# Optimization experiments

Hardware: AMD Instinct MI355X
Metric: run time of the kernel (lower is better)

The kernel has to match this reference:

```python
import jax, jax.numpy as jnp
import numpy as np

N, E, G = 100000, 400000, 64
IN, H, C = 8, 4, 64
HD = H * C  # 256


def setup_inputs() -> dict:
    key = jax.random.key(0)
    ks = jax.random.split(key, 40)
    f = lambda k, shp, s=0.05: jax.random.normal(k, shp, jnp.float32) * s
    inp = {
        "x": jax.random.normal(ks[0], (N, IN), jnp.float32),
        "edge_attr": jax.random.normal(ks[1], (E, 1), jnp.float32),
        "src": jax.random.randint(ks[2], (E,), 0, N),
        "dst": jax.random.randint(ks[3], (E,), 0, N),
        "batch": jnp.sort(jax.random.randint(ks[4], (N,), 0, G)),
        # encoder Linear(8 -> 64)
        "W_enc": f(ks[5], (IN, C)), "b_enc": jnp.zeros((C,), jnp.float32),
        # GATv2 layer 1: in 64 -> H*C=256
        "g1_Wl": f(ks[6], (C, HD)), "g1_bl": jnp.zeros((HD,), jnp.float32),
        "g1_Wr": f(ks[7], (C, HD)), "g1_br": jnp.zeros((HD,), jnp.float32),
        "g1_We": f(ks[8], (1, HD)),
        "g1_att": f(ks[9], (H, C)),
        "g1_bias": jnp.zeros((HD,), jnp.float32),
        # GATv2 layer 2: in 256 -> 256
        "g2_Wl": f(ks[10], (HD, HD)), "g2_bl": jnp.zeros((HD,), jnp.float32),
        "g2_Wr": f(ks[11], (HD, HD)), "g2_br": jnp.zeros((HD,), jnp.float32),
        "g2_We": f(ks[12], (1, HD)),
        "g2_att": f(ks[13], (H, C)),
        "g2_bias": jnp.zeros((HD,), jnp.float32),
        # post MLP: 256 -> 128 -> LN -> relu -> 128 -> 64 -> relu, head 64 -> 1
        "W_p1": f(ks[14], (HD, 128)), "b_p1": jnp.zeros((128,), jnp.float32),
        "ln_g": jnp.ones((128,), jnp.float32), "ln_b": jnp.zeros((128,), jnp.float32),
        "W_p2": f(ks[15], (128, 64)), "b_p2": jnp.zeros((64,), jnp.float32),
        "W_head": f(ks[16], (64, 1)), "b_head": jnp.zeros((1,), jnp.float32),
    }
    return inp


def gatv2(x, src, dst, e_attr, Wl, bl, Wr, br, We, att, bias):
    """PyG GATv2Conv: score = att . LeakyReLU(xl[src] + xr[dst] + e), scatter-softmax over dst,
    out_i = sum_j alpha_ij * xl[j], concat heads, + bias."""
    n = x.shape[0]
    xl = (x @ Wl + bl).reshape(n, H, C)          # source-side transform
    xr = (x @ Wr + br).reshape(n, H, C)          # target-side transform
    ee = (e_attr @ We).reshape(-1, H, C)         # [E,H,C]
    s = jax.nn.leaky_relu(xl[src] + xr[dst] + ee, 0.2)
    logit = jnp.einsum('ehc,hc->eh', s, att)     # [E,H]
    # numerically-stable scatter softmax over edges sharing a target node
    m = jax.ops.segment_max(logit, dst, num_segments=n)
    m = jnp.where(jnp.isfinite(m), m, 0.0)
    ex = jnp.exp(logit - m[dst])
    den = jax.ops.segment_sum(ex, dst, num_segments=n)
    alpha = ex / (den[dst] + 1e-16)
    out = jax.ops.segment_sum(alpha[:, :, None] * xl[src], dst, num_segments=n)
    return out.reshape(n, HD) + bias


def reference(x, edge_attr, src, dst, batch,
              W_enc, b_enc,
              g1_Wl, g1_bl, g1_Wr, g1_br, g1_We, g1_att, g1_bias,
              g2_Wl, g2_bl, g2_Wr, g2_br, g2_We, g2_att, g2_bias,
              W_p1, b_p1, ln_g, ln_b, W_p2, b_p2, W_head, b_head):
    h = jax.nn.relu(x @ W_enc + b_enc)
    h = jax.nn.relu(gatv2(h, src, dst, edge_attr, g1_Wl, g1_bl, g1_Wr, g1_br, g1_We, g1_att, g1_bias))
    h = jax.nn.relu(gatv2(h, src, dst, edge_attr, g2_Wl, g2_bl, g2_Wr, g2_br, g2_We, g2_att, g2_bias))
    # global mean pool per graph
    sums = jax.ops.segment_sum(h, batch, num_segments=G)
    cnt = jax.ops.segment_sum(jnp.ones((h.shape[0],), h.dtype), batch, num_segments=G)
    p = sums / jnp.maximum(cnt, 1.0)[:, None]
    # post MLP (dropout is identity at inference)
    p = p @ W_p1 + b_p1
    mu = jnp.mean(p, axis=-1, keepdims=True)
    var = jnp.mean((p - mu) ** 2, axis=-1, keepdims=True)
    p = (p - mu) * jax.lax.rsqrt(var + 1e-5) * ln_g + ln_b
    p = jax.nn.relu(p)
    p = jax.nn.relu(p @ W_p2 + b_p2)
    return (p @ W_head + b_head)[:, 0]  # [G]
```

## Files before the change

### kernel.cpp

```cpp
#include <hip/hip_runtime.h>
#include <hip/hip_fp16.h>
#include <math.h>


#define HD 256
#define NHEAD 4
#define CH 64

typedef _Float16 half8 __attribute__((ext_vector_type(8)));
typedef _Float16 h2 __attribute__((ext_vector_type(2)));
typedef __attribute__((ext_vector_type(4))) float f32x4;

__device__ __forceinline__ h2 pack_h2(float a, float b) {
#if __has_builtin(__builtin_amdgcn_cvt_pkrtz)
    return __builtin_bit_cast(h2, __builtin_amdgcn_cvt_pkrtz(a, b));
#else
    return h2{(_Float16)a, (_Float16)b};
#endif
}

__device__ __forceinline__ float fast_exp2(float x) {
#if __has_builtin(__builtin_amdgcn_exp2f)
    return __builtin_amdgcn_exp2f(x);
#else
    return exp2f(x);
#endif
}

__device__ __forceinline__ float dot2f(h2 a, h2 b, float c) {
#if __has_builtin(__builtin_amdgcn_fdot2)
    typedef __fp16 fp16v2 __attribute__((ext_vector_type(2)));
    return __builtin_amdgcn_fdot2(__builtin_bit_cast(fp16v2, a),
                                  __builtin_bit_cast(fp16v2, b), c, false);
#else
    return c + (float)a.x * (float)b.x + (float)a.y * (float)b.y;
#endif
}

__device__ __forceinline__ void prep_one(const float* Wl, const float* Wr,
                                         ushort* frag, int K, int t) {
    int l = t & 63;
    int ct = (t >> 6) & 31;
    int ks = t >> 11;
    int n = l & 15, q = l >> 4;
    const float* W = (ct < 16) ? Wl : Wr;
    int col = (ct & 15) * 16 + n;
    ushort* phi = frag + (size_t)t * 8;
#pragma unroll
    for (int j = 0; j < 8; ++j) {
        int k = ks * 32 + q * 8 + j;
        float wv = W[(size_t)k * 256 + col];
        phi[j] = __half_as_ushort(__float2half(wv));
    }
}

__global__ void setup_kernel(int* __restrict__ zbase, int nzero,
                             const float* __restrict__ Wl1, const float* __restrict__ Wr1,
                             ushort* __restrict__ f1,
                             const float* __restrict__ Wl2, const float* __restrict__ Wr2,
                             ushort* __restrict__ f2) {
    int i = blockIdx.x * 256 + threadIdx.x;
    if (i < nzero) {
        zbase[i] = 0;
    } else {
        int gt = i - nzero;
        if (gt < 64 * 64) prep_one(Wl1, Wr1, f1, 64, gt);
        else if (gt < 64 * 64 + 256 * 64) prep_one(Wl2, Wr2, f2, 256, gt - 64 * 64);
    }
}

__global__ void deg_kernel(const int* __restrict__ dst, int* __restrict__ cnt, int E) {
    int e = blockIdx.x * 256 + threadIdx.x;
    if (e < E) atomicAdd(&cnt[dst[e]], 1);
}

__global__ void scan_block(const int* __restrict__ cnt, int* __restrict__ off,
                           int* __restrict__ bsum, int N) {
    __shared__ int s[256];
    int i = blockIdx.x * 256 + threadIdx.x;
    int v = (i < N) ? cnt[i] : 0;
    s[threadIdx.x] = v;
    __syncthreads();
    for (int d = 1; d < 256; d <<= 1) {
        int t = 0;
        if (threadIdx.x >= d) t = s[threadIdx.x - d];
        __syncthreads();
        s[threadIdx.x] += t;
        __syncthreads();
    }
    if (i < N) off[i + 1] = s[threadIdx.x];
    if (threadIdx.x == 255) bsum[blockIdx.x] = s[255];
    if (blockIdx.x == 0 && threadIdx.x == 0) off[0] = 0;
}

__global__ void scan_add2(int* __restrict__ off, const int* __restrict__ bsum, int N) {
    __shared__ int red[4];
    int b = blockIdx.x;
    int s = 0;
    for (int i = threadIdx.x; i < b; i += 256) s += bsum[i];
    for (int o = 32; o > 0; o >>= 1) s += __shfl_xor(s, o);
    if ((threadIdx.x & 63) == 0) red[threadIdx.x >> 6] = s;
    __syncthreads();
    int prefix = red[0] + red[1] + red[2] + red[3];
    int i = b * 256 + threadIdx.x;
    if (i < N) off[i + 1] += prefix;
}

__global__ void scatter_kernel(const int* __restrict__ dst, const int* __restrict__ src,
                               const float* __restrict__ eattr, const int* __restrict__ off,
                               int* __restrict__ cur, int2* __restrict__ edata, int E) {
    int e = blockIdx.x * 256 + threadIdx.x;
    if (e < E) {
        int d = dst[e];
        int p = atomicAdd(&cur[d], 1);
        edata[off[d] + p] = make_int2(src[e] << 9, __float_as_int(eattr[e]));
    }
}

template <int K, bool FUSE_ENC>
__global__ __launch_bounds__(512, 4) void gemm_mfma(
    const void* Av, const float* __restrict__ Wenc, const float* __restrict__ benc,
    const ushort* __restrict__ Bfrag,
    const float* __restrict__ bl, const float* __restrict__ br,
    ushort* __restrict__ outL, ushort* outR, int N) {
    constexpr int KS = K / 32;
    constexpr int FRAG_SHORTS = KS * 4 * 64 * 8;
    constexpr int TB_STRIDE = 260;
    constexpr int SH_BYTES = (FRAG_SHORTS * 2 > 64 * TB_STRIDE * 2)
                                 ? FRAG_SHORTS * 2 : 64 * TB_STRIDE * 2;
    __shared__ __align__(16) char shraw[SH_BYTES];
    ushort* frag = (ushort*)shraw;
    ushort* tbuf = (ushort*)shraw;

    const int t = threadIdx.x;
    const int row0 = blockIdx.x * 64;
    const float* Ax = (const float*)Av;
    const ushort* Ahalf = (const ushort*)Av;

    const int w = t >> 6, l = t & 63;

    if constexpr (FUSE_ENC) {
        constexpr int C4 = K / 4;
        constexpr int LC4 = 4;
#pragma unroll
        for (int it = 0; it < (64 * C4) / 512; ++it) {
            int jj = it * 512 + t;
            int m = jj & 15;
            int c4 = (jj >> 4) & (C4 - 1);
            int rg = jj >> (4 + LC4);
            int row = row0 + rg * 16 + m;
            ushort4 sv = make_ushort4(0, 0, 0, 0);
            if (row < N) {
                float4 xa = *(const float4*)(Ax + (size_t)row * 8);
                float4 xb = *(const float4*)(Ax + (size_t)row * 8 + 4);
                float xrv[8] = {xa.x, xa.y, xa.z, xa.w, xb.x, xb.y, xb.z, xb.w};
                ushort o[4];
#pragma unroll
                for (int j = 0; j < 4; ++j) {
                    int c = c4 * 4 + j;
                    float a = benc[c];
#pragma unroll
                    for (int u = 0; u < 8; ++u) a = fmaf(xrv[u], Wenc[u * 64 + c], a);
                    o[j] = __half_as_ushort(__float2half(fmaxf(a, 0.f)));
                }
                sv = make_ushort4(o[0], o[1], o[2], o[3]);
            }
            int c = c4 * 4;
            int ks = c >> 5, q = (c >> 3) & 3, jb = c & 7;
            int cell = (ks * 4 + rg) * 64 + m + 16 * q;
            *(ushort4*)(frag + cell * 8 + jb) = sv;
        }
    } else {
#if __has_builtin(__builtin_amdgcn_global_load_lds)
#pragma unroll
        for (int it = 0; it < 4; ++it) {
            int row = row0 + it * 16 + (l & 15);
            const ushort* srcp = Ahalf + (size_t)row * 256 + w * 32 + (l >> 4) * 8;
            ushort* dstp = frag + (size_t)(w * 4 + it) * 64 * 8;
            if (row < N) {
                __builtin_amdgcn_global_load_lds(
                    (const __attribute__((address_space(1))) unsigned int*)srcp,
                    (__attribute__((address_space(3))) unsigned int*)dstp,
                    16, 0, 0);
            }
        }
#else
        constexpr int C8 = K / 8;
        constexpr int LC8 = 5;
#pragma unroll
        for (int it = 0; it < (64 * C8) / 512; ++it) {
            int jj = it * 512 + t;
            int m = jj & 15;
            int c8 = (jj >> 4) & (C8 - 1);
            int rg = jj >> (4 + LC8);
            int row = row0 + rg * 16 + m;
            uint4 sv = make_uint4(0, 0, 0, 0);
            if (row < N) sv = *(const uint4*)(Ahalf + (size_t)row * K + c8 * 8);
            int ks = c8 >> 2, q = c8 & 3;
            int cell = (ks * 4 + rg) * 64 + m + 16 * q;
            *(uint4*)(frag + cell * 8) = sv;
        }
#endif
    }
    __syncthreads();

    const int ct0 = w * 4;

    f32x4 acc[4][4];
#pragma unroll
    for (int rt = 0; rt < 4; ++rt)
#pragma unroll
        for (int c = 0; c < 4; ++c) acc[rt][c] = (f32x4){0.f, 0.f, 0.f, 0.f};

#pragma unroll
    for (int ks = 0; ks < KS; ++ks) {
        half8 a[4];
#pragma unroll
        for (int rt = 0; rt < 4; ++rt) {
            int cell = (ks * 4 + rt) * 64 + l;
            a[rt] = *(const half8*)(frag + cell * 8);
        }
#pragma unroll
        for (int c = 0; c < 4; ++c) {
            size_t e = ((size_t)(ks * 32 + ct0 + c) * 64 + l) * 8;
            half8 bh = *(const half8*)(Bfrag + e);
#pragma unroll
            for (int rt = 0; rt < 4; ++rt)
                acc[rt][c] = __builtin_amdgcn_mfma_f32_16x16x32_f16(a[rt], bh, acc[rt][c], 0, 0, 0);
        }
    }

    const int m = l & 15, q = l >> 4;
#pragma unroll
    for (int half = 0; half < 2; ++half) {
        __syncthreads();
        if ((w >> 2) == half) {
            const float* bias = half ? br : bl;
#pragma unroll
            for (int c = 0; c < 4; ++c) {
                int col = ((ct0 + c) & 15) * 16 + m;
                float bb = bias[col];
#pragma unroll
                for (int rt = 0; rt < 4; ++rt)
#pragma unroll
                    for (int r = 0; r < 4; ++r)
                        tbuf[(rt * 16 + q * 4 + r) * TB_STRIDE + col] =
                            __half_as_ushort(__float2half(acc[rt][c][r] + bb));
            }
        }
        __syncthreads();
        ushort* outp = half ? outR : outL;
#pragma unroll
        for (int it = 0; it < 4; ++it) {
            int jj = it * 512 + t;
            int row = jj >> 5;
            int ch = jj & 31;
            int grow = row0 + row;
            if (grow < N) {
                uint2 a0 = *(const uint2*)(tbuf + row * TB_STRIDE + ch * 8);
                uint2 a1 = *(const uint2*)(tbuf + row * TB_STRIDE + ch * 8 + 4);
                *(uint4*)(outp + (size_t)grow * 256 + ch * 8) =
                    make_uint4(a0.x, a0.y, a1.x, a1.y);
            }
        }
    }
}

__global__ __launch_bounds__(256) void gat_aggregate(
    const ushort* __restrict__ xl, const ushort* xr,
    const int* __restrict__ off, const int2* __restrict__ edata,
    const float* __restrict__ We, const float* __restrict__ att,
    const float* __restrict__ bias, ushort* out, int N) {
    const int wid = blockIdx.x * 4 + (threadIdx.x >> 6);
    if (wid * 2 >= N) return;
    const int lane = threadIdx.x & 63;
    const int l32 = lane & 31;
    const int node = wid * 2 + (lane >> 5);
    const int cbase = (l32 >> 3) * 64 + (l32 & 7) * 8;
    const unsigned cb2 = (unsigned)cbase * 2;

    const float LOG2E = 1.44269504f;
    float4 wf0 = *(const float4*)(We + cbase);
    float4 wf1 = *(const float4*)(We + cbase + 4);
    float4 af0 = *(const float4*)(att + cbase);
    float4 af1 = *(const float4*)(att + cbase + 4);
    h2 we[4], at[4];
    we[0] = pack_h2(wf0.x, wf0.y); we[1] = pack_h2(wf0.z, wf0.w);
    we[2] = pack_h2(wf1.x, wf1.y); we[3] = pack_h2(wf1.z, wf1.w);
    at[0] = pack_h2(af0.x * LOG2E, af0.y * LOG2E);
    at[1] = pack_h2(af0.z * LOG2E, af0.w * LOG2E);
    at[2] = pack_h2(af1.x * LOG2E, af1.y * LOG2E);
    at[3] = pack_h2(af1.z * LOG2E, af1.w * LOG2E);

    const h2 z2 = {(_Float16)0.f, (_Float16)0.f};
    const h2 c02 = {(_Float16)0.2f, (_Float16)0.2f};

    const bool valid = node < N;
    const size_t nb = (size_t)node * HD;
    h2 xrv[4] = {z2, z2, z2, z2};
    int s0i = 0, s1i = 0;
    if (valid) {
        uint4 xu = *(const uint4*)(xr + nb + cbase);
        xrv[0] = __builtin_bit_cast(h2, xu.x);
        xrv[1] = __builtin_bit_cast(h2, xu.y);
        xrv[2] = __builtin_bit_cast(h2, xu.z);
        xrv[3] = __builtin_bit_cast(h2, xu.w);
        s0i = off[node];
        s1i = off[node + 1];
    }

    const char* xlb = (const char*)xl;
    const char* eb = (const char*)edata;
    float l = 0.f;
    h2 acc[4] = {z2, z2, z2, z2};

    int j[4];
    float ea[4];
    {
        unsigned tb = (unsigned)s0i << 3;
        int2 e0 = *(const int2*)(eb + tb);
        int2 e1 = *(const int2*)(eb + tb + 8);
        int2 e2 = *(const int2*)(eb + tb + 16);
        int2 e3 = *(const int2*)(eb + tb + 24);
        j[0] = e0.x; ea[0] = __int_as_float(e0.y);
        j[1] = e1.x; ea[1] = __int_as_float(e1.y);
        j[2] = e2.x; ea[2] = __int_as_float(e2.y);
        j[3] = e3.x; ea[3] = __int_as_float(e3.y);
    }
    int t = s0i;
    while (__any(t < s1i)) {
        int nE = s1i - t;
        int jc[4];
        float eac[4];
#pragma unroll
        for (int u = 0; u < 4; ++u) { jc[u] = j[u]; eac[u] = ea[u]; }
        h2 xv[4][4];
#pragma unroll
        for (int u = 0; u < 4; ++u) {
            unsigned a = (u < nE) ? (unsigned)jc[u] : 0u;
            uint4 xu = *(const uint4*)(xlb + (a + cb2));
            xv[u][0] = __builtin_bit_cast(h2, xu.x);
            xv[u][1] = __builtin_bit_cast(h2, xu.y);
            xv[u][2] = __builtin_bit_cast(h2, xu.z);
            xv[u][3] = __builtin_bit_cast(h2, xu.w);
        }
        {
            unsigned tb = (unsigned)(t + 4) << 3;
            int2 e0 = *(const int2*)(eb + tb);
            int2 e1 = *(const int2*)(eb + tb + 8);
            int2 e2 = *(const int2*)(eb + tb + 16);
            int2 e3 = *(const int2*)(eb + tb + 24);
            j[0] = e0.x; ea[0] = __int_as_float(e0.y);
            j[1] = e1.x; ea[1] = __int_as_float(e1.y);
            j[2] = e2.x; ea[2] = __int_as_float(e2.y);
            j[3] = e3.x; ea[3] = __int_as_float(e3.y);
        }
        float rr[4];
#pragma unroll
        for (int u = 0; u < 4; ++u) {
            _Float16 eh = (_Float16)eac[u];
            h2 e2 = {eh, eh};
            float v = 0.f;
#pragma unroll
            for (int k = 0; k < 4; ++k) {
                h2 s = e2 * we[k] + (xv[u][k] + xrv[k]);
                s = __builtin_elementwise_max(s, z2) + __builtin_elementwise_min(s, z2) * c02;
                v = dot2f(at[k], s, v);
            }
            rr[u] = v;
        }
        h2 r01 = pack_h2(rr[0], rr[1]);
        h2 r23 = pack_h2(rr[2], rr[3]);
#pragma unroll
        for (int o = 1; o <= 4; o <<= 1) {
            int v01 = __shfl_xor(__builtin_bit_cast(int, r01), o);
            int v23 = __shfl_xor(__builtin_bit_cast(int, r23), o);
            r01 = r01 + __builtin_bit_cast(h2, v01);
            r23 = r23 + __builtin_bit_cast(h2, v23);
        }
        float r0 = (float)r01.x, r1 = (float)r01.y;
        float r2 = (float)r23.x, r3 = (float)r23.y;
        if (0 >= nE) r0 = -1e30f;
        if (1 >= nE) r1 = -1e30f;
        if (2 >= nE) r2 = -1e30f;
        if (3 >= nE) r3 = -1e30f;
        float p0 = fast_exp2(r0);
        float p1 = fast_exp2(r1);
        float p2 = fast_exp2(r2);
        float p3 = fast_exp2(r3);
        l += (p0 + p1) + (p2 + p3);
        h2 ph0 = pack_h2(p0, p0);
        h2 ph1 = pack_h2(p1, p1);
        h2 ph2 = pack_h2(p2, p2);
        h2 ph3 = pack_h2(p3, p3);
#pragma unroll
        for (int k = 0; k < 4; ++k) {
            acc[k] = ph0 * xv[0][k] + acc[k];
            acc[k] = ph1 * xv[1][k] + acc[k];
            acc[k] = ph2 * xv[2][k] + acc[k];
            acc[k] = ph3 * xv[3][k] + acc[k];
        }
        t += 4;
    }
    if (valid) {
        float inv = 1.f / (l + 1e-16f);
        float4 b0 = *(const float4*)(bias + cbase);
        float4 b1 = *(const float4*)(bias + cbase + 4);
        float q0 = fmaxf(fmaf((float)acc[0].x, inv, b0.x), 0.f);
        float q1 = fmaxf(fmaf((float)acc[0].y, inv, b0.y), 0.f);
        float q2 = fmaxf(fmaf((float)acc[1].x, inv, b0.z), 0.f);
        float q3 = fmaxf(fmaf((float)acc[1].y, inv, b0.w), 0.f);
        float q4 = fmaxf(fmaf((float)acc[2].x, inv, b1.x), 0.f);
        float q5 = fmaxf(fmaf((float)acc[2].y, inv, b1.y), 0.f);
        float q6 = fmaxf(fmaf((float)acc[3].x, inv, b1.z), 0.f);
        float q7 = fmaxf(fmaf((float)acc[3].y, inv, b1.w), 0.f);
        uint w0 = (uint)__half_as_ushort(__float2half(q0)) |
                  ((uint)__half_as_ushort(__float2half(q1)) << 16);
        uint w1 = (uint)__half_as_ushort(__float2half(q2)) |
                  ((uint)__half_as_ushort(__float2half(q3)) << 16);
        uint w2 = (uint)__half_as_ushort(__float2half(q4)) |
                  ((uint)__half_as_ushort(__float2half(q5)) << 16);
        uint w3 = (uint)__half_as_ushort(__float2half(q6)) |
                  ((uint)__half_as_ushort(__float2half(q7)) << 16);
        *(uint4*)(out + nb + cbase) = make_uint4(w0, w1, w2, w3);
    }
}

__device__ __forceinline__ int lowerb(const int* b, int n, int v) {
    int lo = 0, hi = n;
    while (lo < hi) {
        int mid = (lo + hi) >> 1;
        if (b[mid] < v) lo = mid + 1; else hi = mid;
    }
    return lo;
}

__global__ __launch_bounds__(256) void pool_kernel(
    const ushort* __restrict__ h, const int* __restrict__ batch,
    float* __restrict__ pooled, float* __restrict__ gcnt, int N) {
    const int g = blockIdx.x >> 5, part = blockIdx.x & 31;
    const int start = lowerb(batch, N, g);
    const int end = lowerb(batch, N, g + 1);
    const int rows = end - start;
    const int r0 = start + (int)((long long)rows * part / 32);
    const int r1 = start + (int)((long long)rows * (part + 1) / 32);

    const int slot = threadIdx.x >> 5;
    const int l32 = threadIdx.x & 31;

    float acc[8] = {0.f, 0.f, 0.f, 0.f, 0.f, 0.f, 0.f, 0.f};
    for (int r = r0 + slot; r < r1; r += 8) {
        uint4 v = *(const uint4*)(h + (size_t)r * HD + l32 * 8);
        h2 a0 = __builtin_bit_cast(h2, v.x);
        h2 a1 = __builtin_bit_cast(h2, v.y);
        h2 a2 = __builtin_bit_cast(h2, v.z);
        h2 a3 = __builtin_bit_cast(h2, v.w);
        acc[0] += (float)a0.x; acc[1] += (float)a0.y;
        acc[2] += (float)a1.x; acc[3] += (float)a1.y;
        acc[4] += (float)a2.x; acc[5] += (float)a2.y;
        acc[6] += (float)a3.x; acc[7] += (float)a3.y;
    }
#pragma unroll
    for (int k = 0; k < 8; ++k) acc[k] += __shfl_xor(acc[k], 32);

    __shared__ float sred[4][32][9];
    const int w = threadIdx.x >> 6;
    if ((threadIdx.x & 63) < 32) {
#pragma unroll
        for (int k = 0; k < 8; ++k) sred[w][l32][k] = acc[k];
    }
    __syncthreads();
    {
        const int li = threadIdx.x >> 3;
        const int k = threadIdx.x & 7;
        float s = (sred[0][li][k] + sred[1][li][k]) +
                  (sred[2][li][k] + sred[3][li][k]);
        atomicAdd(&pooled[g * HD + li * 8 + k], s);
    }
    if (part == 0 && threadIdx.x == 0) gcnt[g] = (float)rows;
}

__global__ void mlp_kernel(const float* __restrict__ pooled, const float* __restrict__ gcnt,
                           const float* __restrict__ W_p1, const float* __restrict__ b_p1,
                           const float* __restrict__ ln_g, const float* __restrict__ ln_b,
                           const float* __restrict__ W_p2, const float* __restrict__ b_p2,
                           const float* __restrict__ W_head, const float* __restrict__ b_head,
                           float* __restrict__ out) {
    int g = blockIdx.x;
    int j = threadIdx.x;
    __shared__ float sh[128];
    __shared__ float red[2];

    float inv = 1.f / fmaxf(gcnt[g], 1.f);
    float v = b_p1[j];
    for (int k = 0; k < 256; ++k) v = fmaf(pooled[g * 256 + k] * inv, W_p1[k * 128 + j], v);

    float s = v;
    for (int o = 32; o > 0; o >>= 1) s += __shfl_xor(s, o);
    if ((j & 63) == 0) red[j >> 6] = s;
    __syncthreads();
    float mu = (red[0] + red[1]) * (1.f / 128.f);
    float d = v - mu;
    float s2 = d * d;
    for (int o = 32; o > 0; o >>= 1) s2 += __shfl_xor(s2, o);
    __syncthreads();
    if ((j & 63) == 0) red[j >> 6] = s2;
    __syncthreads();
    float var = (red[0] + red[1]) * (1.f / 128.f);

    float p = d * rsqrtf(var + 1e-5f) * ln_g[j] + ln_b[j];
    sh[j] = fmaxf(p, 0.f);
    __syncthreads();

    if (j < 64) {
        float q = b_p2[j];
        for (int k = 0; k < 128; ++k) q = fmaf(sh[k], W_p2[k * 64 + j], q);
        q = fmaxf(q, 0.f);
        float t = q * W_head[j];
        for (int o = 32; o > 0; o >>= 1) t += __shfl_xor(t, o);
        if (j == 0) out[g] = t + b_head[0];
    }
}

extern "C" void kernel_launch(void* const* d_in, const int* in_sizes, int n_in,
                              void* d_out, int out_size, void* d_ws, size_t ws_size,
                              hipStream_t stream) {
    const float* x      = (const float*)d_in[0];
    const float* eattr  = (const float*)d_in[1];
    const int*   src    = (const int*)d_in[2];
    const int*   dst    = (const int*)d_in[3];
    const int*   batch  = (const int*)d_in[4];
    const float* W_enc  = (const float*)d_in[5];
    const float* b_enc  = (const float*)d_in[6];
    const float* g1_Wl  = (const float*)d_in[7];
    const float* g1_bl  = (const float*)d_in[8];
    const float* g1_Wr  = (const float*)d_in[9];
    const float* g1_br  = (const float*)d_in[10];
    const float* g1_We  = (const float*)d_in[11];
    const float* g1_att = (const float*)d_in[12];
    const float* g1_bias= (const float*)d_in[13];
    const float* g2_Wl  = (const float*)d_in[14];
    const float* g2_bl  = (const float*)d_in[15];
    const float* g2_Wr  = (const float*)d_in[16];
    const float* g2_br  = (const float*)d_in[17];
    const float* g2_We  = (const float*)d_in[18];
    const float* g2_att = (const float*)d_in[19];
    const float* g2_bias= (const float*)d_in[20];
    const float* W_p1   = (const float*)d_in[21];
    const float* b_p1   = (const float*)d_in[22];
    const float* ln_g   = (const float*)d_in[23];
    const float* ln_b   = (const float*)d_in[24];
    const float* W_p2   = (const float*)d_in[25];
    const float* b_p2   = (const float*)d_in[26];
    const float* W_head = (const float*)d_in[27];
    const float* b_head = (const float*)d_in[28];

    const int N = in_sizes[0] / 8;
    const int E = in_sizes[2];

    char* p = (char*)d_ws;
    auto alloc = [&](size_t bytes) -> void* {
        void* r = (void*)p;
        p += (bytes + 255) & ~(size_t)255;
        return r;
    };
    ushort* bufA   = (ushort*)alloc((size_t)N * HD * 2);
    ushort* bufXL  = (ushort*)alloc((size_t)N * HD * 2);
    int*    cnt    = (int*)alloc((size_t)N * 4);
    int*    curp   = (int*)alloc((size_t)N * 4);
    float*  pooled = (float*)alloc(64 * HD * 4);
    char*   zend   = p;
    int*    off    = (int*)alloc((size_t)(N + 1) * 4);
    int2*   edata  = (int2*)alloc((size_t)(E + 8) * 8);
    const int nb   = (N + 255) / 256;
    int*    bsum   = (int*)alloc((size_t)nb * 4);
    float*  gcnt   = (float*)alloc(64 * 4);
    ushort* wfrag1 = (ushort*)alloc((size_t)64 * 64 * 16 * 2);
    ushort* wfrag2 = (ushort*)alloc((size_t)256 * 64 * 16 * 2);

    const int nzero = (int)(((char*)zend - (char*)cnt) / 4);
    const int nsetup = nzero + 64 * 64 + 256 * 64;

    setup_kernel<<<(nsetup + 255) / 256, 256, 0, stream>>>(
        cnt, nzero, g1_Wl, g1_Wr, wfrag1, g2_Wl, g2_Wr, wfrag2);

    deg_kernel<<<(E + 255) / 256, 256, 0, stream>>>(dst, cnt, E);
    scan_block<<<nb, 256, 0, stream>>>(cnt, off, bsum, N);
    scan_add2<<<nb, 256, 0, stream>>>(off, bsum, N);
    scatter_kernel<<<(E + 255) / 256, 256, 0, stream>>>(dst, src, eattr, off, curp,
                                                        edata, E);

    const int gblocks = (N + 63) / 64;
    const int ablocks = (N + 7) / 8;

    gemm_mfma<64, true><<<gblocks, 512, 0, stream>>>(
        x, W_enc, b_enc, wfrag1, g1_bl, g1_br, bufXL, bufA, N);
    gat_aggregate<<<ablocks, 256, 0, stream>>>(
        bufXL, bufA, off, edata, g1_We, g1_att, g1_bias, bufA, N);

    gemm_mfma<256, false><<<gblocks, 512, 0, stream>>>(
        bufA, nullptr, nullptr, wfrag2, g2_bl, g2_br, bufXL, bufA, N);
    gat_aggregate<<<ablocks, 256, 0, stream>>>(
        bufXL, bufA, off, edata, g2_We, g2_att, g2_bias, bufA, N);

    pool_kernel<<<64 * 32, 256, 0, stream>>>(bufA, batch, pooled, gcnt, N);
    mlp_kernel<<<64, 128, 0, stream>>>(pooled, gcnt, W_p1, b_p1, ln_g, ln_b,
                                       W_p2, b_p2, W_head, b_head, (float*)d_out);
}
```

Before: 358.0 us.

## Sort nodes by in-degree to balance edges across aggregate wavefronts

Adds a counting sort of nodes by in-degree (histogram, scan, scatter into a permutation), and the GAT aggregation kernels process nodes in that permuted order. Each wavefront handles two nodes on half-waves, so pairing nodes of similar degree is meant to cut divergence and idle lanes from degree imbalance. The cost is three extra small kernels plus an indirection through perm, which makes the xr reads and output writes non-contiguous across neighbouring waves and can hurt coalescing and cache locality.

```diff
diff --git a/kernel.cpp b/kernel.cpp
--- a/kernel.cpp
+++ b/kernel.cpp
@@ -115,6 +115,42 @@
         int p = atomicAdd(&cur[d], 1);
         edata[off[d] + p] = make_int2(src[e] << 9, __float_as_int(eattr[e]));
     }
+}
+
+__global__ void dhist_kernel(const int* __restrict__ cnt, int* __restrict__ dhist, int N) {
+    __shared__ int lh[64];
+    if (threadIdx.x < 64) lh[threadIdx.x] = 0;
+    __syncthreads();
+    int i = blockIdx.x * 256 + threadIdx.x;
+    if (i < N) atomicAdd(&lh[min(cnt[i], 63)], 1);
+    __syncthreads();
+    if (threadIdx.x < 64 && lh[threadIdx.x] > 0)
+        atomicAdd(&dhist[threadIdx.x], lh[threadIdx.x]);
+}
+
+__global__ void dscan_kernel(const int* __restrict__ dhist, int* __restrict__ dcur) {
+    if (threadIdx.x == 0) {
+        int a = 0;
+        for (int k = 0; k < 64; ++k) { dcur[k] = a; a += dhist[k]; }
+    }
+}
+
+__global__ void sort_scatter(const int* __restrict__ cnt, int* __restrict__ dcur,
+                             int* __restrict__ perm, int N) {
+    __shared__ int lh[64], lbase[64];
+    if (threadIdx.x < 64) lh[threadIdx.x] = 0;
+    __syncthreads();
+    int i = blockIdx.x * 256 + threadIdx.x;
+    int bin = 0, r = 0;
+    if (i < N) {
+        bin = min(cnt[i], 63);
+        r = atomicAdd(&lh[bin], 1);
+    }
+    __syncthreads();
+    if (threadIdx.x < 64 && lh[threadIdx.x] > 0)
+        lbase[threadIdx.x] = atomicAdd(&dcur[threadIdx.x], lh[threadIdx.x]);
+    __syncthreads();
+    if (i < N) perm[lbase[bin] + r] = i;
 }
 
 template <int K, bool FUSE_ENC>
@@ -269,13 +305,14 @@
 __global__ __launch_bounds__(256) void gat_aggregate(
     const ushort* __restrict__ xl, const ushort* xr,
     const int* __restrict__ off, const int2* __restrict__ edata,
+    const int* __restrict__ perm,
     const float* __restrict__ We, const float* __restrict__ att,
     const float* __restrict__ bias, ushort* out, int N) {
     const int wid = blockIdx.x * 4 + (threadIdx.x >> 6);
     if (wid * 2 >= N) return;
     const int lane = threadIdx.x & 63;
     const int l32 = lane & 31;
-    const int node = wid * 2 + (lane >> 5);
+    const int idx = wid * 2 + (lane >> 5);
     const int cbase = (l32 >> 3) * 64 + (l32 & 7) * 8;
     const unsigned cb2 = (unsigned)cbase * 2;
 
@@ -295,7 +332,9 @@
     const h2 z2 = {(_Float16)0.f, (_Float16)0.f};
     const h2 c02 = {(_Float16)0.2f, (_Float16)0.2f};
 
-    const bool valid = node < N;
+    const bool valid = idx < N;
+    int node = 0;
+    if (valid) node = perm[idx];
     const size_t nb = (size_t)node * HD;
     h2 xrv[4] = {z2, z2, z2, z2};
     int s0i = 0, s1i = 0;
@@ -568,6 +607,7 @@
     ushort* bufXL  = (ushort*)alloc((size_t)N * HD * 2);
     int*    cnt    = (int*)alloc((size_t)N * 4);
     int*    curp   = (int*)alloc((size_t)N * 4);
+    int*    dhist  = (int*)alloc(64 * 4);
     float*  pooled = (float*)alloc(64 * HD * 4);
     char*   zend   = p;
     int*    off    = (int*)alloc((size_t)(N + 1) * 4);
@@ -575,6 +615,8 @@
     const int nb   = (N + 255) / 256;
     int*    bsum   = (int*)alloc((size_t)nb * 4);
     float*  gcnt   = (float*)alloc(64 * 4);
+    int*    dcur   = (int*)alloc(64 * 4);
+    int*    perm   = (int*)alloc((size_t)N * 4);
     ushort* wfrag1 = (ushort*)alloc((size_t)64 * 64 * 16 * 2);
     ushort* wfrag2 = (ushort*)alloc((size_t)256 * 64 * 16 * 2);
 
@@ -585,8 +627,11 @@
         cnt, nzero, g1_Wl, g1_Wr, wfrag1, g2_Wl, g2_Wr, wfrag2);
 
     deg_kernel<<<(E + 255) / 256, 256, 0, stream>>>(dst, cnt, E);
+    dhist_kernel<<<nb, 256, 0, stream>>>(cnt, dhist, N);
+    dscan_kernel<<<1, 64, 0, stream>>>(dhist, dcur);
     scan_block<<<nb, 256, 0, stream>>>(cnt, off, bsum, N);
     scan_add2<<<nb, 256, 0, stream>>>(off, bsum, N);
+    sort_scatter<<<nb, 256, 0, stream>>>(cnt, dcur, perm, N);
     scatter_kernel<<<(E + 255) / 256, 256, 0, stream>>>(dst, src, eattr, off, curp,
                                                         edata, E);
 
@@ -596,12 +641,12 @@
     gemm_mfma<64, true><<<gblocks, 512, 0, stream>>>(
         x, W_enc, b_enc, wfrag1, g1_bl, g1_br, bufXL, bufA, N);
     gat_aggregate<<<ablocks, 256, 0, stream>>>(
-        bufXL, bufA, off, edata, g1_We, g1_att, g1_bias, bufA, N);
+        bufXL, bufA, off, edata, perm, g1_We, g1_att, g1_bias, bufA, N);
 
     gemm_mfma<256, false><<<gblocks, 512, 0, stream>>>(
         bufA, nullptr, nullptr, wfrag2, g2_bl, g2_br, bufXL, bufA, N);
     gat_aggregate<<<ablocks, 256, 0, stream>>>(
-        bufXL, bufA, off, edata, g2_We, g2_att, g2_bias, bufA, N);
+        bufXL, bufA, off, edata, perm, g2_We, g2_att, g2_bias, bufA, N);
 
     pool_kernel<<<64 * 32, 256, 0, stream>>>(bufA, batch, pooled, gcnt, N);
     mlp_kernel<<<64, 128, 0, stream>>>(pooled, gcnt, W_p1, b_p1, ln_g, ln_b,
```

Result: slower. 377.3 us (+5.4%).

## Add 32-row MFMA GEMM kernel for layer-2 transform with wider column tiles

Applied to the files above, without the earlier changes.

Replaces the layer-2 GEMM (256->512 outputs) with a dedicated kernel that processes 32 rows per block using 256 threads. Each wave computes 8 column tiles over 2 row tiles, so each B fragment loaded from global memory feeds two MFMAs. The kernel writes both the left and right halves in a single epilogue pass. The intent is to double the grid size and shrink per-block shared memory for better occupancy and latency hiding, at the cost of more B-fragment traffic per output row. The generic kernel's non-fused branch is removed since only the fused-encoder instantiation remains.

```diff
diff --git a/kernel.cpp b/kernel.cpp
--- a/kernel.cpp
+++ b/kernel.cpp
@@ -135,11 +135,10 @@
     const int t = threadIdx.x;
     const int row0 = blockIdx.x * 64;
     const float* Ax = (const float*)Av;
-    const ushort* Ahalf = (const ushort*)Av;
 
     const int w = t >> 6, l = t & 63;
 
-    if constexpr (FUSE_ENC) {
+    {
         constexpr int C4 = K / 4;
         constexpr int LC4 = 4;
 #pragma unroll
@@ -170,37 +169,6 @@
             int cell = (ks * 4 + rg) * 64 + m + 16 * q;
             *(ushort4*)(frag + cell * 8 + jb) = sv;
         }
-    } else {
-#if __has_builtin(__builtin_amdgcn_global_load_lds)
-#pragma unroll
-        for (int it = 0; it < 4; ++it) {
-            int row = row0 + it * 16 + (l & 15);
-            const ushort* srcp = Ahalf + (size_t)row * 256 + w * 32 + (l >> 4) * 8;
-            ushort* dstp = frag + (size_t)(w * 4 + it) * 64 * 8;
-            if (row < N) {
-                __builtin_amdgcn_global_load_lds(
-                    (const __attribute__((address_space(1))) unsigned int*)srcp,
-                    (__attribute__((address_space(3))) unsigned int*)dstp,
-                    16, 0, 0);
-            }
-        }
-#else
-        constexpr int C8 = K / 8;
-        constexpr int LC8 = 5;
-#pragma unroll
-        for (int it = 0; it < (64 * C8) / 512; ++it) {
-            int jj = it * 512 + t;
-            int m = jj & 15;
-            int c8 = (jj >> 4) & (C8 - 1);
-            int rg = jj >> (4 + LC8);
-            int row = row0 + rg * 16 + m;
-            uint4 sv = make_uint4(0, 0, 0, 0);
-            if (row < N) sv = *(const uint4*)(Ahalf + (size_t)row * K + c8 * 8);
-            int ks = c8 >> 2, q = c8 & 3;
-            int cell = (ks * 4 + rg) * 64 + m + 16 * q;
-            *(uint4*)(frag + cell * 8) = sv;
-        }
-#endif
     }
     __syncthreads();
 
@@ -262,6 +230,105 @@
                 *(uint4*)(outp + (size_t)grow * 256 + ch * 8) =
                     make_uint4(a0.x, a0.y, a1.x, a1.y);
             }
+        }
+    }
+}
+
+__global__ __launch_bounds__(256, 4) void gemm_mfma32(
+    const ushort* __restrict__ A, const ushort* __restrict__ Bfrag,
+    const float* __restrict__ bl, const float* __restrict__ br,
+    ushort* __restrict__ outL, ushort* outR, int N) {
+    constexpr int TB_STRIDE = 516;
+    constexpr int SH_BYTES = 32 * TB_STRIDE * 2;
+    __shared__ __align__(16) char shraw[SH_BYTES];
+    ushort* frag = (ushort*)shraw;
+    ushort* tbuf = (ushort*)shraw;
+
+    const int t = threadIdx.x;
+    const int row0 = blockIdx.x * 32;
+    const int w = t >> 6, l = t & 63;
+
+#if __has_builtin(__builtin_amdgcn_global_load_lds)
+#pragma unroll
+    for (int it = 0; it < 4; ++it) {
+        int cb = w * 4 + it;
+        int ks = cb >> 1, rg = cb & 1;
+        int row = row0 + rg * 16 + (l & 15);
+        const ushort* srcp = A + (size_t)row * 256 + ks * 32 + (l >> 4) * 8;
+        ushort* dstp = frag + (size_t)cb * 512;
+        if (row < N) {
+            __builtin_amdgcn_global_load_lds(
+                (const __attribute__((address_space(1))) unsigned int*)srcp,
+                (__attribute__((address_space(3))) unsigned int*)dstp,
+                16, 0, 0);
+        }
+    }
+#else
+#pragma unroll
+    for (int it = 0; it < 4; ++it) {
+        int cb = w * 4 + it;
+        int ks = cb >> 1, rg = cb & 1;
+        int row = row0 + rg * 16 + (l & 15);
+        uint4 sv = make_uint4(0, 0, 0, 0);
+        if (row < N) sv = *(const uint4*)(A + (size_t)row * 256 + ks * 32 + (l >> 4) * 8);
+        *(uint4*)(frag + (size_t)cb * 512 + l * 8) = sv;
+    }
+#endif
+    __syncthreads();
+
+    f32x4 acc[2][8];
+#pragma unroll
+    for (int rt = 0; rt < 2; ++rt)
+#pragma unroll
+        for (int c = 0; c < 8; ++c) acc[rt][c] = (f32x4){0.f, 0.f, 0.f, 0.f};
+
+#pragma unroll
+    for (int ks = 0; ks < 8; ++ks) {
+        half8 a0 = *(const half8*)(frag + ((ks * 2 + 0) * 64 + l) * 8);
+        half8 a1 = *(const half8*)(frag + ((ks * 2 + 1) * 64 + l) * 8);
+#pragma unroll
+        for (int ch_ = 0; ch_ < 2; ++ch_) {
+#pragma unroll
+            for (int cc = 0; cc < 4; ++cc) {
+                int c = ch_ * 4 + cc;
+                int ct = w * 8 + c;
+                size_t e = ((size_t)(ks * 32 + ct) * 64 + l) * 8;
+                half8 bh = *(const half8*)(Bfrag + e);
+                acc[0][c] = __builtin_amdgcn_mfma_f32_16x16x32_f16(a0, bh, acc[0][c], 0, 0, 0);
+                acc[1][c] = __builtin_amdgcn_mfma_f32_16x16x32_f16(a1, bh, acc[1][c], 0, 0, 0);
+            }
+        }
+    }
+    __syncthreads();
+
+    const int m = l & 15, q = l >> 4;
+#pragma unroll
+    for (int c = 0; c < 8; ++c) {
+        int ct = w * 8 + c;
+        int col = ct * 16 + m;
+        float bb = (ct < 16) ? bl[col] : br[col - 256];
+#pragma unroll
+        for (int rt = 0; rt < 2; ++rt)
+#pragma unroll
+            for (int r = 0; r < 4; ++r)
+                tbuf[(rt * 16 + q * 4 + r) * TB_STRIDE + col] =
+                    __half_as_ushort(__float2half(acc[rt][c][r] + bb));
+    }
+    __syncthreads();
+
+#pragma unroll
+    for (int it = 0; it < 8; ++it) {
+        int jj = it * 256 + t;
+        int row = jj >> 6;
+        int ch = jj & 63;
+        int grow = row0 + row;
+        if (grow < N) {
+            ushort* outp = (ch < 32) ? outL : outR;
+            int cc = (ch & 31) * 8;
+            uint2 a0 = *(const uint2*)(tbuf + row * TB_STRIDE + ch * 8);
+            uint2 a1 = *(const uint2*)(tbuf + row * TB_STRIDE + ch * 8 + 4);
+            *(uint4*)(outp + (size_t)grow * 256 + cc) =
+                make_uint4(a0.x, a0.y, a1.x, a1.y);
         }
     }
 }
@@ -591,6 +658,7 @@
                                                         edata, E);
 
     const int gblocks = (N + 63) / 64;
+    const int g32blocks = (N + 31) / 32;
     const int ablocks = (N + 7) / 8;
 
     gemm_mfma<64, true><<<gblocks, 512, 0, stream>>>(
@@ -598,8 +666,8 @@
     gat_aggregate<<<ablocks, 256, 0, stream>>>(
         bufXL, bufA, off, edata, g1_We, g1_att, g1_bias, bufA, N);
 
-    gemm_mfma<256, false><<<gblocks, 512, 0, stream>>>(
-        bufA, nullptr, nullptr, wfrag2, g2_bl, g2_br, bufXL, bufA, N);
+    gemm_mfma32<<<g32blocks, 256, 0, stream>>>(
+        bufA, wfrag2, g2_bl, g2_br, bufXL, bufA, N);
     gat_aggregate<<<ablocks, 256, 0, stream>>>(
         bufXL, bufA, off, edata, g2_We, g2_att, g2_bias, bufA, N);
 
```

Measured after the change: 396.1 us. 10.6% more time.
